# Optimization experiments

Measured on AMD Instinct MI355X. Metric: run time of the kernel, lower is better.

The kernel has to match this reference:

```python
import jax, jax.numpy as jnp
import numpy as np

NEG_SLOPE = 0.2  # PyG GATConv default negative_slope
N_NODES = 50000


def gat_conv(x, src, dst, W, att_src, att_dst, bias, heads, out_ch):
    # x: [N, F_in]; src/dst: [E] (messages flow src -> dst, softmax over dst)
    N = x.shape[0]
    h = (x @ W).reshape(N, heads, out_ch)              # [N,H,C]
    a_src = jnp.sum(h * att_src, axis=-1)              # [N,H]
    a_dst = jnp.sum(h * att_dst, axis=-1)              # [N,H]
    e = jax.nn.leaky_relu(a_src[src] + a_dst[dst], NEG_SLOPE)   # [E,H]
    # numerically stable segment softmax over incoming edges of each dst node
    m = jax.ops.segment_max(e, dst, num_segments=N)    # [N,H]
    e = jnp.exp(e - m[dst])
    denom = jax.ops.segment_sum(e, dst, num_segments=N)
    alpha = e / (denom[dst] + 1e-16)                   # [E,H]
    msg = h[src] * alpha[:, :, None]                   # [E,H,C]
    out = jax.ops.segment_sum(msg, dst, num_segments=N)  # [N,H,C]
    return out.reshape(N, heads * out_ch) + bias


def add_self_loops(edge_index, num_nodes):
    loop = jnp.arange(num_nodes, dtype=edge_index.dtype)
    return jnp.concatenate([edge_index, jnp.stack([loop, loop])], axis=1)


def setup_inputs() -> dict:
    key = jax.random.key(0)
    ks = jax.random.split(key, 10)
    F_in, H, C, F_out = 256, 4, 64, 16
    x = jax.random.normal(ks[0], (N_NODES, F_in), dtype=jnp.float32)
    edge_index = jax.random.randint(ks[1], (2, 800000), 0, N_NODES, dtype=jnp.int64)
    s1 = 1.0 / np.sqrt(F_in)
    s2 = 1.0 / np.sqrt(H * C)
    return {
        "x": x,
        "edge_index": edge_index,
        "W1": jax.random.normal(ks[2], (F_in, H * C), dtype=jnp.float32) * s1,
        "att_src1": jax.random.normal(ks[3], (H, C), dtype=jnp.float32) * s2,
        "att_dst1": jax.random.normal(ks[4], (H, C), dtype=jnp.float32) * s2,
        "b1": jnp.zeros((H * C,), dtype=jnp.float32),
        "W2": jax.random.normal(ks[5], (H * C, F_out), dtype=jnp.float32) * s2,
        "att_src2": jax.random.normal(ks[6], (1, F_out), dtype=jnp.float32) * 0.25,
        "att_dst2": jax.random.normal(ks[7], (1, F_out), dtype=jnp.float32) * 0.25,
        "b2": jnp.zeros((F_out,), dtype=jnp.float32),
    }


def reference(x, edge_index, W1, att_src1, att_dst1, b1, W2, att_src2, att_dst2, b2):
    ei = add_self_loops(edge_index, x.shape[0])
    src, dst = ei[0], ei[1]
    H1, C1 = att_src1.shape
    h = gat_conv(x, src, dst, W1, att_src1, att_dst1, b1, H1, C1)
    h = jax.nn.relu(h)
    # F.dropout(training=False) is identity in eval mode
    H2, C2 = att_src2.shape
    out = gat_conv(h, src, dst, W2, att_src2, att_dst2, b2, H2, C2)
    return jax.nn.log_softmax(out, axis=1)
```

## Files before the change

kernel.cpp:

```cpp
#include <hip/hip_runtime.h>
#include <math.h>


typedef __attribute__((ext_vector_type(8))) short bf16x8;
typedef __attribute__((ext_vector_type(8))) unsigned short u16x8;
typedef __attribute__((ext_vector_type(4))) float f32x4;
typedef __attribute__((ext_vector_type(2))) float f32x2;

#define BCAP 1536

static __device__ inline unsigned short f2bf(float f) {
    unsigned u = __builtin_bit_cast(unsigned, f);
    unsigned r = (u + 0x7FFF + ((u >> 16) & 1)) >> 16;
    return (unsigned short)r;
}
static __device__ inline float bf2f(unsigned short u) {
    unsigned v = ((unsigned)u) << 16;
    return __builtin_bit_cast(float, v);
}
static __device__ inline float lrelu(float x) { return x > 0.f ? x : 0.2f * x; }

__global__ __launch_bounds__(256) void k_prep_w1t(const float* __restrict__ W1,
                                                  short* __restrict__ w1t,
                                                  int* __restrict__ fill_bkt,
                                                  int nbuk) {
    int idx = blockIdx.x * 256 + threadIdx.x;
    if (idx < nbuk) fill_bkt[idx] = 0;
    int n = idx >> 8, k = idx & 255;
    w1t[n * 256 + k] = (short)f2bf(W1[k * 256 + n]);
}

__global__ __launch_bounds__(256) void k_bucketize(const int* __restrict__ ei,
                                                   int* __restrict__ fill_bkt,
                                                   uint2* __restrict__ tmp,
                                                   int E0, int nbuk) {
    __shared__ int hist[1024];
    __shared__ int base[1024];
    const int t = threadIdx.x;
    const int e0 = blockIdx.x * 4096;
    for (int b = t; b < nbuk; b += 256) hist[b] = 0;
    __syncthreads();
    int ss[16], ds[16];
    int nm = 0;
#pragma unroll
    for (int k = 0; k < 16; ++k) {
        int e = e0 + t + k * 256;
        if (e < E0) {
            ss[nm] = ei[e];
            ds[nm] = ei[E0 + e];
            atomicAdd(&hist[ds[nm] >> 6], 1);
            ++nm;
        }
    }
    __syncthreads();
    for (int b = t; b < nbuk; b += 256) {
        int c = hist[b];
        base[b] = c ? atomicAdd(&fill_bkt[b], c) : 0;
        hist[b] = 0;
    }
    __syncthreads();
    for (int k = 0; k < nm; ++k) {
        int b = ds[k] >> 6;
        int r = base[b] + atomicAdd(&hist[b], 1);
        if (r < BCAP) tmp[(long)b * BCAP + r] = make_uint2((unsigned)ss[k], (unsigned)ds[k]);
    }
}

__global__ __launch_bounds__(256) void k_build_deg(const uint2* __restrict__ tmp,
                                                   const int* __restrict__ fill_bkt,
                                                   int* __restrict__ deg, int N) {
    __shared__ int hist[64];
    const int b = blockIdx.x;
    const int t = threadIdx.x;
    if (t < 64) hist[t] = 0;
    __syncthreads();
    int cnt = min(fill_bkt[b], BCAP);
    const uint2* tp = tmp + (long)b * BCAP;
    for (int i = t; i < cnt; i += 256)
        atomicAdd(&hist[tp[i].y & 63], 1);
    __syncthreads();
    if (t < 64) {
        int d = b * 64 + t;
        if (d < N) deg[d] = hist[t] + 1;
    }
}

__global__ __launch_bounds__(1024) void k_scan1(const int* __restrict__ deg,
                                                int* __restrict__ off,
                                                int* __restrict__ bsum, int N) {
    __shared__ int s[1024];
    int t = threadIdx.x;
    int i = blockIdx.x * 1024 + t;
    int v = (i < N) ? deg[i] : 0;
    s[t] = v;
    __syncthreads();
    for (int o = 1; o < 1024; o <<= 1) {
        int tv = (t >= o) ? s[t - o] : 0;
        __syncthreads();
        s[t] += tv;
        __syncthreads();
    }
    if (i < N) off[i] = s[t] - v;
    if (t == 1023) bsum[blockIdx.x] = s[1023];
}

__global__ __launch_bounds__(256) void k_scan3(int* __restrict__ off,
                                               const int* __restrict__ bsum,
                                               int N, int Etot, int NB) {
    __shared__ int pbs[64];
    int t = threadIdx.x;
    if (t < 64) {
        int v = (t < NB) ? bsum[t] : 0;
        for (int o = 1; o < 64; o <<= 1) {
            int u = __shfl_up(v, o);
            if (t >= o) v += u;
        }
        pbs[t] = v;
    }
    __syncthreads();
    int i = blockIdx.x * 256 + t;
    if (i < N) {
        int blk = i >> 10;
        off[i] += blk ? pbs[blk - 1] : 0;
    }
    if (i == 0) off[N] = Etot;
}

__global__ __launch_bounds__(256) void k_csr_fill(const uint2* __restrict__ tmp,
                                                  const int* __restrict__ fill_bkt,
                                                  const int* __restrict__ off,
                                                  int* __restrict__ csr, int N) {
    __shared__ int loff[64];
    __shared__ int lfill[64];
    const int b = blockIdx.x;
    const int t = threadIdx.x;
    if (t < 64) {
        int d = b * 64 + t;
        loff[t] = (d < N) ? off[d] : 0;
        lfill[t] = 0;
    }
    __syncthreads();
    int cnt = min(fill_bkt[b], BCAP);
    const uint2* tp = tmp + (long)b * BCAP;
    for (int i = t; i < cnt; i += 256) {
        uint2 e = tp[i];
        int dl = e.y & 63;
        int r = atomicAdd(&lfill[dl], 1);
        csr[loff[dl] + r] = (int)e.x;
    }
    __syncthreads();
    if (t < 64) {
        int d = b * 64 + t;
        if (d < N) csr[loff[t] + lfill[t]] = d;
    }
}

__global__ __launch_bounds__(256) void k_gemm1_mfma(const float* __restrict__ A,
                                                    const short* __restrict__ Bt,
                                                    const float* __restrict__ att_s,
                                                    const float* __restrict__ att_d,
                                                    unsigned char* __restrict__ C8,
                                                    float* __restrict__ a1s,
                                                    float* __restrict__ a1d,
                                                    int M) {
    __shared__ short As[128][40];
    __shared__ short Bs[128][40];
    const int bm = blockIdx.y * 128;
    const int bn = blockIdx.x * 128;
    const int tid = threadIdx.x;
    const int lane = tid & 63;
    const int wave = tid >> 6;
    const int wm = (wave >> 1) * 64;
    const int wn = (wave & 1) * 64;
    const int l15 = lane & 15;
    const int l4 = lane >> 4;

    const int sr = tid >> 1;
    const int sh = (tid & 1) * 16;

    f32x4 acc[4][4] = {};

    for (int k0 = 0; k0 < 256; k0 += 32) {
        {
            float v[16];
            if (bm + sr < M) {
                const float* p = &A[(long)(bm + sr) * 256 + k0 + sh];
#pragma unroll
                for (int q = 0; q < 4; ++q) {
                    float4 fv = *(const float4*)(p + q * 4);
                    v[q * 4 + 0] = fv.x; v[q * 4 + 1] = fv.y;
                    v[q * 4 + 2] = fv.z; v[q * 4 + 3] = fv.w;
                }
            } else {
#pragma unroll
                for (int q = 0; q < 16; ++q) v[q] = 0.f;
            }
            short b[16];
#pragma unroll
            for (int q = 0; q < 16; ++q) b[q] = (short)f2bf(v[q]);
            *(bf16x8*)&As[sr][sh] = *(bf16x8*)&b[0];
            *(bf16x8*)&As[sr][sh + 8] = *(bf16x8*)&b[8];
        }
        {
            const short* p = &Bt[(long)(bn + sr) * 256 + k0 + sh];
            bf16x8 b0 = *(const bf16x8*)p;
            bf16x8 b1 = *(const bf16x8*)(p + 8);
            *(bf16x8*)&Bs[sr][sh] = b0;
            *(bf16x8*)&Bs[sr][sh + 8] = b1;
        }
        __syncthreads();

        bf16x8 af[4], bfr[4];
#pragma unroll
        for (int i = 0; i < 4; ++i)
            af[i] = *(const bf16x8*)&As[wm + i * 16 + l15][l4 * 8];
#pragma unroll
        for (int j = 0; j < 4; ++j)
            bfr[j] = *(const bf16x8*)&Bs[wn + j * 16 + l15][l4 * 8];
#pragma unroll
        for (int i = 0; i < 4; ++i)
#pragma unroll
            for (int j = 0; j < 4; ++j)
                acc[i][j] = __builtin_amdgcn_mfma_f32_16x16x32_bf16(af[i], bfr[j], acc[i][j], 0, 0, 0);
        __syncthreads();
    }

    const int h = (bn + wn) >> 6;
    float aws[4], awd[4];
#pragma unroll
    for (int j = 0; j < 4; ++j) {
        aws[j] = att_s[h * 64 + j * 16 + l15];
        awd[j] = att_d[h * 64 + j * 16 + l15];
    }

#pragma unroll
    for (int i = 0; i < 4; ++i) {
#pragma unroll
        for (int r = 0; r < 4; ++r) {
            float sv = 0.f, dv = 0.f;
#pragma unroll
            for (int j = 0; j < 4; ++j) {
                sv += acc[i][j][r] * aws[j];
                dv += acc[i][j][r] * awd[j];
            }
#pragma unroll
            for (int o = 1; o < 16; o <<= 1) {
                sv += __shfl_xor(sv, o);
                dv += __shfl_xor(dv, o);
            }
            int row = bm + wm + i * 16 + l4 * 4 + r;
            if (row < M) {
                if (l15 == 0) { a1s[row * 4 + h] = sv; a1d[row * 4 + h] = dv; }
#pragma unroll
                for (int j = 0; j < 4; ++j) {
                    float vv = acc[i][j][r];
                    C8[(long)row * 256 + bn + wn + j * 16 + l15] =
                        (unsigned char)(__builtin_amdgcn_cvt_pk_fp8_f32(vv, vv, 0, false) & 0xFF);
                }
            }
        }
    }
}

__global__ __launch_bounds__(256) void k_expden1(const int* __restrict__ off,
                                                 const int* __restrict__ csr,
                                                 const float* __restrict__ as1,
                                                 const float* __restrict__ ad1,
                                                 float* __restrict__ alphaE,
                                                 float* __restrict__ dinv, int N) {
    int wid = blockIdx.x * 4 + (threadIdx.x >> 6);
    int lane = threadIdx.x & 63;
    if (wid >= N) return;
    int begin = off[wid], end = off[wid + 1];
    int h = lane >> 4, t = lane & 15;
    float adh = ad1[wid * 4 + h];
    float den = 0.f;
    for (int j = begin + t; j < end; j += 16) {
        float ex = __expf(lrelu(as1[csr[j] * 4 + h] + adh));
        alphaE[j * 4 + h] = ex;
        den += ex;
    }
#pragma unroll
    for (int o = 1; o < 16; o <<= 1) den += __shfl_xor(den, o);
    if (t == 0) dinv[wid * 4 + h] = 1.f / (den + 1e-16f);
}

__global__ __launch_bounds__(256) void k_gather1(const unsigned char* __restrict__ h1f8,
                                                 const int* __restrict__ off,
                                                 const int* __restrict__ csr,
                                                 const float* __restrict__ alphaE,
                                                 const float* __restrict__ dinv,
                                                 const float* __restrict__ b1,
                                                 unsigned short* __restrict__ out1b,
                                                 int N) {
    int wid = blockIdx.x * 4 + (threadIdx.x >> 6);
    int lane = threadIdx.x & 63;
    if (wid >= N) return;
    int begin = off[wid], end = off[wid + 1];
    const int es = lane >> 4;
    const int cl = lane & 15;
    float acc[16] = {};
#pragma unroll 2
    for (int j0 = begin; j0 < end; j0 += 4) {
        int j = j0 + es;
        bool valid = j < end;
        int jc = valid ? j : begin;
        int s = csr[jc];
        float a = valid ? alphaE[jc * 4 + (cl >> 2)] : 0.f;
        uint4 v = *(const uint4*)&h1f8[(long)s * 256 + cl * 16];
        unsigned w[4] = {v.x, v.y, v.z, v.w};
#pragma unroll
        for (int q = 0; q < 4; ++q) {
            f32x2 lo = __builtin_amdgcn_cvt_pk_f32_fp8((int)w[q], false);
            f32x2 hi = __builtin_amdgcn_cvt_pk_f32_fp8((int)w[q], true);
            acc[q * 4 + 0] += a * lo.x;
            acc[q * 4 + 1] += a * lo.y;
            acc[q * 4 + 2] += a * hi.x;
            acc[q * 4 + 3] += a * hi.y;
        }
    }
#pragma unroll
    for (int q = 0; q < 16; ++q) {
        acc[q] += __shfl_xor(acc[q], 16);
        acc[q] += __shfl_xor(acc[q], 32);
    }
    if (lane < 16) {
        float inv = dinv[wid * 4 + (cl >> 2)];
        unsigned pk[8];
#pragma unroll
        for (int q = 0; q < 8; ++q) {
            float v0 = fmaxf(acc[q * 2 + 0] * inv + b1[cl * 16 + q * 2 + 0], 0.f);
            float v1 = fmaxf(acc[q * 2 + 1] * inv + b1[cl * 16 + q * 2 + 1], 0.f);
            pk[q] = (unsigned)f2bf(v0) | ((unsigned)f2bf(v1) << 16);
        }
        unsigned short* dst = &out1b[(long)wid * 256 + cl * 16];
        *(uint4*)dst = make_uint4(pk[0], pk[1], pk[2], pk[3]);
        *(uint4*)(dst + 8) = make_uint4(pk[4], pk[5], pk[6], pk[7]);
    }
}

__global__ __launch_bounds__(256) void k_gemm2(const unsigned short* __restrict__ Xb,
                                               const float* __restrict__ W,
                                               const float* __restrict__ att_s,
                                               const float* __restrict__ att_d,
                                               float* __restrict__ h2,
                                               float* __restrict__ a2s,
                                               float* __restrict__ a2d, int N) {
    __shared__ float Ws[256 * 16];
    for (int i = threadIdx.x; i < 1024; i += 256)
        ((float4*)Ws)[i] = ((const float4*)W)[i];
    __syncthreads();
    int r = threadIdx.x >> 4, c = threadIdx.x & 15;
    int row = blockIdx.x * 16 + r;
    if (row >= N) return;
    const unsigned short* xr = Xb + (long)row * 256;
    float acc = 0.f;
    for (int k = 0; k < 256; k += 8) {
        u16x8 xv = *(const u16x8*)&xr[k];
#pragma unroll
        for (int q = 0; q < 8; ++q) acc += bf2f(xv[q]) * Ws[(k + q) * 16 + c];
    }
    h2[row * 16 + c] = acc;
    float vs = acc * att_s[c];
    float vd = acc * att_d[c];
    for (int o = 1; o < 16; o <<= 1) { vs += __shfl_xor(vs, o); vd += __shfl_xor(vd, o); }
    if (c == 0) { a2s[row] = vs; a2d[row] = vd; }
}

__global__ __launch_bounds__(256) void k_gather2(const float* __restrict__ h2,
                                                 const int* __restrict__ off,
                                                 const int* __restrict__ csr,
                                                 const float* __restrict__ a2s,
                                                 const float* __restrict__ a2d,
                                                 const float* __restrict__ b2,
                                                 float* __restrict__ out, int N) {
    int wid = blockIdx.x * 4 + (threadIdx.x >> 6);
    int lane = threadIdx.x & 63;
    if (wid >= N) return;
    int begin = off[wid], end = off[wid + 1];
    float adh = a2d[wid];
    float den = 0.f;
    for (int j = begin + lane; j < end; j += 64)
        den += __expf(lrelu(a2s[csr[j]] + adh));
#pragma unroll
    for (int o = 32; o; o >>= 1) den += __shfl_xor(den, o);
    float inv = 1.f / (den + 1e-16f);
    const int es = lane >> 4;
    const int c = lane & 15;
    float acc = 0.f;
#pragma unroll 2
    for (int j0 = begin; j0 < end; j0 += 4) {
        int j = j0 + es;
        bool valid = j < end;
        int jc = valid ? j : begin;
        int s = csr[jc];
        float a = valid ? __expf(lrelu(a2s[s] + adh)) : 0.f;
        acc += a * h2[(long)s * 16 + c];
    }
    acc += __shfl_xor(acc, 16);
    acc += __shfl_xor(acc, 32);
    float v = acc * inv + b2[c];
    float mx = v;
    for (int o = 1; o < 16; o <<= 1) mx = fmaxf(mx, __shfl_xor(mx, o));
    float se = __expf(v - mx);
    for (int o = 1; o < 16; o <<= 1) se += __shfl_xor(se, o);
    float r = v - mx - logf(se);
    if (lane < 16) out[(long)wid * 16 + c] = r;
}

extern "C" void kernel_launch(void* const* d_in, const int* in_sizes, int n_in,
                              void* d_out, int out_size, void* d_ws, size_t ws_size,
                              hipStream_t stream) {
    const float* x    = (const float*)d_in[0];
    const int*   ei   = (const int*)d_in[1];
    const float* W1   = (const float*)d_in[2];
    const float* as1w = (const float*)d_in[3];
    const float* ad1w = (const float*)d_in[4];
    const float* b1   = (const float*)d_in[5];
    const float* W2   = (const float*)d_in[6];
    const float* as2w = (const float*)d_in[7];
    const float* ad2w = (const float*)d_in[8];
    const float* b2   = (const float*)d_in[9];
    float* out = (float*)d_out;

    const int N    = in_sizes[0] / 256;
    const int E0   = in_sizes[1] / 2;
    const int Etot = E0 + N;
    const int NB   = (N + 1023) / 1024;
    const int NBUK = (N + 63) >> 6;

    char* p = (char*)d_ws;
    unsigned char*  h1f8  = (unsigned char*)p;  p += (size_t)N * 256;
    unsigned short* out1b = (unsigned short*)p; p += (size_t)N * 256 * sizeof(short);
    float* h2     = (float*)p; p += (size_t)N * 16 * sizeof(float);
    float* a1s    = (float*)p; p += (size_t)N * 4 * sizeof(float);
    float* a1d    = (float*)p; p += (size_t)N * 4 * sizeof(float);
    float* a2s    = (float*)p; p += (size_t)N * sizeof(float);
    float* a2d    = (float*)p; p += (size_t)N * sizeof(float);
    float* alphaE = (float*)p; p += (size_t)Etot * 4 * sizeof(float);
    float* dinv   = (float*)p; p += (size_t)N * 4 * sizeof(float);
    int*   deg    = (int*)p;   p += (size_t)N * sizeof(int);
    int*   off    = (int*)p;   p += (size_t)(N + 1) * sizeof(int);
    int*   bsum   = (int*)p;   p += (size_t)64 * sizeof(int);
    int*   fillbk = (int*)p;   p += (size_t)NBUK * sizeof(int);
    short* w1t    = (short*)p; p += (size_t)256 * 256 * sizeof(short);
    int*   csr    = (int*)p;   p += (size_t)Etot * sizeof(int);
    uint2* tmp    = (uint2*)p; p += (size_t)NBUK * BCAP * sizeof(uint2);

    const int NW = (N + 3) / 4;

    hipLaunchKernelGGL(k_prep_w1t, dim3(256), dim3(256), 0, stream, W1, w1t, fillbk, NBUK);

    hipLaunchKernelGGL(k_bucketize, dim3((E0 + 4095) / 4096), dim3(256), 0, stream,
                       ei, fillbk, tmp, E0, NBUK);
    hipLaunchKernelGGL(k_build_deg, dim3(NBUK), dim3(256), 0, stream, tmp, fillbk, deg, N);
    hipLaunchKernelGGL(k_scan1, dim3(NB), dim3(1024), 0, stream, deg, off, bsum, N);
    hipLaunchKernelGGL(k_scan3, dim3((N + 255) / 256), dim3(256), 0, stream, off, bsum, N, Etot, NB);
    hipLaunchKernelGGL(k_csr_fill, dim3(NBUK), dim3(256), 0, stream, tmp, fillbk, off, csr, N);

    hipLaunchKernelGGL(k_gemm1_mfma, dim3(2, (N + 127) / 128), dim3(256), 0, stream,
                       x, w1t, as1w, ad1w, h1f8, a1s, a1d, N);
    hipLaunchKernelGGL(k_expden1, dim3(NW), dim3(256), 0, stream,
                       off, csr, a1s, a1d, alphaE, dinv, N);
    hipLaunchKernelGGL(k_gather1, dim3(NW), dim3(256), 0, stream,
                       h1f8, off, csr, alphaE, dinv, b1, out1b, N);

    hipLaunchKernelGGL(k_gemm2, dim3((N + 15) / 16), dim3(256), 0, stream,
                       out1b, W2, as2w, ad2w, h2, a2s, a2d, N);
    hipLaunchKernelGGL(k_gather2, dim3(NW), dim3(256), 0, stream,
                       h2, off, csr, a2s, a2d, b2, out, N);
}
```

Baseline: 272.4 us.

## Fuse CSR offset computation into bucket scan and fill, pack gather accumulators

Replaces the four-kernel degree/scan/fill pipeline with a single-block scan over per-bucket edge counts followed by a fill kernel that computes per-node offsets locally with a wave scan. This removes two kernel launches and the deg/bsum round trips through global memory. Separately, the layer-1 gather keeps its accumulators as float2 vectors so the compiler can use packed FMA. The single-block scan only handles up to 1024 buckets (65536 nodes), which limits the supported graph size.

```diff
diff --git a/kernel.cpp b/kernel.cpp
--- a/kernel.cpp
+++ b/kernel.cpp
@@ -66,13 +66,40 @@
     }
 }
 
-__global__ __launch_bounds__(256) void k_build_deg(const uint2* __restrict__ tmp,
-                                                   const int* __restrict__ fill_bkt,
-                                                   int* __restrict__ deg, int N) {
+__global__ __launch_bounds__(1024) void k_bucket_scan(const int* __restrict__ fill_bkt,
+                                                      int* __restrict__ bbase,
+                                                      int* __restrict__ off,
+                                                      int N, int nbuk) {
+    __shared__ int s[1024];
+    int t = threadIdx.x;
+    int cnt = 0;
+    if (t < nbuk) {
+        int nodec = min(64, N - t * 64);
+        cnt = min(fill_bkt[t], BCAP) + nodec;
+    }
+    s[t] = cnt;
+    __syncthreads();
+    for (int o = 1; o < 1024; o <<= 1) {
+        int v = (t >= o) ? s[t - o] : 0;
+        __syncthreads();
+        s[t] += v;
+        __syncthreads();
+    }
+    if (t < nbuk) bbase[t] = s[t] - cnt;
+    if (t == nbuk - 1) { bbase[nbuk] = s[t]; off[N] = s[t]; }
+}
+
+__global__ __launch_bounds__(256) void k_csr_fill(const uint2* __restrict__ tmp,
+                                                  const int* __restrict__ fill_bkt,
+                                                  const int* __restrict__ bbase,
+                                                  int* __restrict__ off,
+                                                  int* __restrict__ csr, int N) {
     __shared__ int hist[64];
+    __shared__ int loff[64];
+    __shared__ int lfill[64];
     const int b = blockIdx.x;
     const int t = threadIdx.x;
-    if (t < 64) hist[t] = 0;
+    if (t < 64) { hist[t] = 0; lfill[t] = 0; }
     __syncthreads();
     int cnt = min(fill_bkt[b], BCAP);
     const uint2* tp = tmp + (long)b * BCAP;
@@ -80,68 +107,19 @@
         atomicAdd(&hist[tp[i].y & 63], 1);
     __syncthreads();
     if (t < 64) {
+        int v = hist[t] + 1;
+        int incl = v;
+#pragma unroll
+        for (int o = 1; o < 64; o <<= 1) {
+            int u = __shfl_up(incl, o);
+            if (t >= (unsigned)o) incl += u;
+        }
+        int lo = bbase[b] + incl - v;
+        loff[t] = lo;
         int d = b * 64 + t;
-        if (d < N) deg[d] = hist[t] + 1;
-    }
-}
-
-__global__ __launch_bounds__(1024) void k_scan1(const int* __restrict__ deg,
-                                                int* __restrict__ off,
-                                                int* __restrict__ bsum, int N) {
-    __shared__ int s[1024];
-    int t = threadIdx.x;
-    int i = blockIdx.x * 1024 + t;
-    int v = (i < N) ? deg[i] : 0;
-    s[t] = v;
-    __syncthreads();
-    for (int o = 1; o < 1024; o <<= 1) {
-        int tv = (t >= o) ? s[t - o] : 0;
-        __syncthreads();
-        s[t] += tv;
-        __syncthreads();
-    }
-    if (i < N) off[i] = s[t] - v;
-    if (t == 1023) bsum[blockIdx.x] = s[1023];
-}
-
-__global__ __launch_bounds__(256) void k_scan3(int* __restrict__ off,
-                                               const int* __restrict__ bsum,
-                                               int N, int Etot, int NB) {
-    __shared__ int pbs[64];
-    int t = threadIdx.x;
-    if (t < 64) {
-        int v = (t < NB) ? bsum[t] : 0;
-        for (int o = 1; o < 64; o <<= 1) {
-            int u = __shfl_up(v, o);
-            if (t >= o) v += u;
-        }
-        pbs[t] = v;
-    }
-    __syncthreads();
-    int i = blockIdx.x * 256 + t;
-    if (i < N) {
-        int blk = i >> 10;
-        off[i] += blk ? pbs[blk - 1] : 0;
-    }
-    if (i == 0) off[N] = Etot;
-}
-
-__global__ __launch_bounds__(256) void k_csr_fill(const uint2* __restrict__ tmp,
-                                                  const int* __restrict__ fill_bkt,
-                                                  const int* __restrict__ off,
-                                                  int* __restrict__ csr, int N) {
-    __shared__ int loff[64];
-    __shared__ int lfill[64];
-    const int b = blockIdx.x;
-    const int t = threadIdx.x;
-    if (t < 64) {
-        int d = b * 64 + t;
-        loff[t] = (d < N) ? off[d] : 0;
-        lfill[t] = 0;
-    }
-    __syncthreads();
-    int cnt = min(fill_bkt[b], BCAP);
-    const uint2* tp = tmp + (long)b * BCAP;
+        if (d < N) off[d] = lo;
+    }
+    __syncthreads();
     for (int i = t; i < cnt; i += 256) {
         uint2 e = tp[i];
         int dl = e.y & 63;
@@ -151,7 +129,7 @@
     __syncthreads();
     if (t < 64) {
         int d = b * 64 + t;
-        if (d < N) csr[loff[t] + lfill[t]] = d;
+        if (d < N) csr[loff[t] + hist[t]] = d;
     }
 }
 
@@ -299,7 +277,7 @@
     int begin = off[wid], end = off[wid + 1];
     const int es = lane >> 4;
     const int cl = lane & 15;
-    float acc[16] = {};
+    f32x2 acc2[8] = {};
 #pragma unroll 2
     for (int j0 = begin; j0 < end; j0 += 4) {
         int j = j0 + es;
@@ -307,30 +285,32 @@
         int jc = valid ? j : begin;
         int s = csr[jc];
         float a = valid ? alphaE[jc * 4 + (cl >> 2)] : 0.f;
+        f32x2 av = {a, a};
         uint4 v = *(const uint4*)&h1f8[(long)s * 256 + cl * 16];
         unsigned w[4] = {v.x, v.y, v.z, v.w};
 #pragma unroll
         for (int q = 0; q < 4; ++q) {
             f32x2 lo = __builtin_amdgcn_cvt_pk_f32_fp8((int)w[q], false);
             f32x2 hi = __builtin_amdgcn_cvt_pk_f32_fp8((int)w[q], true);
-            acc[q * 4 + 0] += a * lo.x;
-            acc[q * 4 + 1] += a * lo.y;
-            acc[q * 4 + 2] += a * hi.x;
-            acc[q * 4 + 3] += a * hi.y;
-        }
-    }
+            acc2[q * 2 + 0] += av * lo;
+            acc2[q * 2 + 1] += av * hi;
+        }
+    }
+    float accf[16];
+#pragma unroll
+    for (int q = 0; q < 8; ++q) { accf[2 * q] = acc2[q].x; accf[2 * q + 1] = acc2[q].y; }
 #pragma unroll
     for (int q = 0; q < 16; ++q) {
-        acc[q] += __shfl_xor(acc[q], 16);
-        acc[q] += __shfl_xor(acc[q], 32);
+        accf[q] += __shfl_xor(accf[q], 16);
+        accf[q] += __shfl_xor(accf[q], 32);
     }
     if (lane < 16) {
         float inv = dinv[wid * 4 + (cl >> 2)];
         unsigned pk[8];
 #pragma unroll
         for (int q = 0; q < 8; ++q) {
-            float v0 = fmaxf(acc[q * 2 + 0] * inv + b1[cl * 16 + q * 2 + 0], 0.f);
-            float v1 = fmaxf(acc[q * 2 + 1] * inv + b1[cl * 16 + q * 2 + 1], 0.f);
+            float v0 = fmaxf(accf[q * 2 + 0] * inv + b1[cl * 16 + q * 2 + 0], 0.f);
+            float v1 = fmaxf(accf[q * 2 + 1] * inv + b1[cl * 16 + q * 2 + 1], 0.f);
             pk[q] = (unsigned)f2bf(v0) | ((unsigned)f2bf(v1) << 16);
         }
         unsigned short* dst = &out1b[(long)wid * 256 + cl * 16];
@@ -426,7 +406,6 @@
     const int N    = in_sizes[0] / 256;
     const int E0   = in_sizes[1] / 2;
     const int Etot = E0 + N;
-    const int NB   = (N + 1023) / 1024;
     const int NBUK = (N + 63) >> 6;
 
     char* p = (char*)d_ws;
@@ -439,9 +418,8 @@
     float* a2d    = (float*)p; p += (size_t)N * sizeof(float);
     float* alphaE = (float*)p; p += (size_t)Etot * 4 * sizeof(float);
     float* dinv   = (float*)p; p += (size_t)N * 4 * sizeof(float);
-    int*   deg    = (int*)p;   p += (size_t)N * sizeof(int);
     int*   off    = (int*)p;   p += (size_t)(N + 1) * sizeof(int);
-    int*   bsum   = (int*)p;   p += (size_t)64 * sizeof(int);
+    int*   bbase  = (int*)p;   p += (size_t)(NBUK + 1) * sizeof(int);
     int*   fillbk = (int*)p;   p += (size_t)NBUK * sizeof(int);
     short* w1t    = (short*)p; p += (size_t)256 * 256 * sizeof(short);
     int*   csr    = (int*)p;   p += (size_t)Etot * sizeof(int);
@@ -453,10 +431,10 @@
 
     hipLaunchKernelGGL(k_bucketize, dim3((E0 + 4095) / 4096), dim3(256), 0, stream,
                        ei, fillbk, tmp, E0, NBUK);
-    hipLaunchKernelGGL(k_build_deg, dim3(NBUK), dim3(256), 0, stream, tmp, fillbk, deg, N);
-    hipLaunchKernelGGL(k_scan1, dim3(NB), dim3(1024), 0, stream, deg, off, bsum, N);
-    hipLaunchKernelGGL(k_scan3, dim3((N + 255) / 256), dim3(256), 0, stream, off, bsum, N, Etot, NB);
-    hipLaunchKernelGGL(k_csr_fill, dim3(NBUK), dim3(256), 0, stream, tmp, fillbk, off, csr, N);
+    hipLaunchKernelGGL(k_bucket_scan, dim3(1), dim3(1024), 0, stream,
+                       fillbk, bbase, off, N, NBUK);
+    hipLaunchKernelGGL(k_csr_fill, dim3(NBUK), dim3(256), 0, stream,
+                       tmp, fillbk, bbase, off, csr, N);
 
     hipLaunchKernelGGL(k_gemm1_mfma, dim3(2, (N + 127) / 128), dim3(256), 0, stream,
                        x, w1t, as1w, ad1w, h1f8, a1s, a1d, N);
```

Result: faster. 264.0 us (-3.1%).
